# Kernel optimization log

Measured on AMD Instinct MI355X. Metric: run time of the kernel, lower is better.

## Reference

```python
import jax, jax.numpy as jnp
import numpy as np

DIM = 128
NUM_HEADS = 16
DPH = DIM // NUM_HEADS
N_ATOMS = 50000
N_EDGES = 400000
LN_EPS = 1e-5


def setup_inputs() -> dict:
    key = jax.random.key(0)
    ks = jax.random.split(key, 12)
    inp = {
        "node_feat": jax.random.normal(ks[0], (N_ATOMS, DIM), jnp.float32),
        "edge_feat": jax.random.normal(ks[1], (N_EDGES, NUM_HEADS, DPH), jnp.float32),
        "edge_vec": jax.random.normal(ks[2], (N_EDGES, 3, 1, 1), jnp.float32),
        "radial": jax.random.uniform(ks[3], (N_EDGES,), jnp.float32),
        "qkv_w": jax.random.normal(ks[4], (DIM, 3 * DIM), jnp.float32) / np.sqrt(DIM),
        "qkv_b": jnp.zeros((3 * DIM,), jnp.float32),
        "out_w": jax.random.normal(ks[5], (DIM, DIM), jnp.float32) / np.sqrt(DIM),
        "out_b": jnp.zeros((DIM,), jnp.float32),
        "ln_g": jnp.ones((DIM,), jnp.float32),
        "ln_b": jnp.zeros((DIM,), jnp.float32),
        "row": jax.random.randint(ks[6], (N_EDGES,), 0, N_ATOMS, jnp.int32),
        "col": jax.random.randint(ks[7], (N_EDGES,), 0, N_ATOMS, jnp.int32),
        "natoms": N_ATOMS,
    }
    return inp


def _layer_norm(x, g, b):
    mu = jnp.mean(x, axis=-1, keepdims=True)
    var = jnp.mean(jnp.square(x - mu), axis=-1, keepdims=True)
    return (x - mu) * jax.lax.rsqrt(var + LN_EPS) * g + b


def reference(node_feat, edge_feat, edge_vec, radial, qkv_w, qkv_b, out_w, out_b,
              ln_g, ln_b, row, col, natoms):
    # LayerNorm + QKV projection (dense)
    h = _layer_norm(node_feat, ln_g, ln_b)                     # [N, D]
    qkv = h @ qkv_w + qkv_b                                    # [N, 3D]
    qkv = qkv.reshape(-1, NUM_HEADS, 3 * DPH)                  # [N, H, 3*Dh]
    q, k, v = qkv[..., :DPH], qkv[..., DPH:2 * DPH], qkv[..., 2 * DPH:]
    # Gather by edge indices
    q_row, k_col, v_col = q[row], k[col], v[col]               # [E, H, Dh]
    # Per-edge attention (exact erf GELU, matching torch nn.GELU default)
    attn = jax.nn.gelu(jnp.sum(q_row * k_col, axis=-1), approximate=False)
    attn = attn * radial[:, None]                              # [E, H]
    # Scalar message + scatter-add
    m_feat = v_col * edge_feat * attn[..., None]               # [E, H, Dh]
    m_feat = jax.ops.segment_sum(m_feat, row, num_segments=natoms)
    m_feat = m_feat.reshape(natoms, DIM)                       # [N, D]
    # Vector message + scatter-add
    m_vec = v_col[:, None, :, :] * edge_vec                    # [E, 3, H, Dh]
    m_vec = jax.ops.segment_sum(m_vec, row, num_segments=natoms)
    delta_node_vec = m_vec.reshape(natoms, 3, DIM)             # [N, 3, D]
    delta_node_feat = m_feat @ out_w + out_b                   # [N, D]
    return delta_node_feat, delta_node_vec
```

## Files before the change

### kernel.cpp

```cpp
#include <hip/hip_runtime.h>
#include <math.h>

#define DIM 128
#define NHEADS 16
#define DPH 8
#define NATOMS 50000
#define NEDGES 400000
#define LN_EPS 1e-5f

typedef float f32x4 __attribute__((ext_vector_type(4)));
typedef short s16x8 __attribute__((ext_vector_type(8)));

static __device__ __forceinline__ unsigned short f2bf(float f) {
  unsigned u = __builtin_bit_cast(unsigned, f);
  unsigned r = (u + 0x7FFFu + ((u >> 16) & 1u)) >> 16;
  return (unsigned short)r;
}
static __device__ __forceinline__ unsigned packbf(float lo, float hi) {
  return (unsigned)f2bf(lo) | ((unsigned)f2bf(hi) << 16);
}
static __device__ __forceinline__ float bflo(unsigned u) {
  return __builtin_bit_cast(float, u << 16);
}
static __device__ __forceinline__ float bfhi(unsigned u) {
  return __builtin_bit_cast(float, u & 0xffff0000u);
}

static __device__ __forceinline__ float gelu_fast(float x) {
  const float c0 = 0.7978845608028654f;
  const float c1 = 0.044715f;
  float u = c0 * (x + c1 * x * x * x);
  return __fdividef(x, 1.0f + __expf(-2.0f * u));
}

#define HIST_NB ((NEDGES + 255) / 256)
#define SCAN_NB 196
#define LN_NB (NATOMS / 16)

__global__ __launch_bounds__(256) void k_convert(
    const float* __restrict__ qkv_w, const float* __restrict__ out_w,
    unsigned short* __restrict__ wTq, unsigned short* __restrict__ wTo,
    int* __restrict__ cnt)
{
  const int idx = blockIdx.x * 256 + threadIdx.x;
  if (idx < NATOMS) cnt[idx] = 0;
  if (idx < 384 * 128) {
    const int c = idx >> 7, k = idx & 127;
    wTq[idx] = f2bf(qkv_w[k * 384 + c]);
  } else {
    const int i2 = idx - 384 * 128;
    const int c = i2 >> 7, k = i2 & 127;
    wTo[i2] = f2bf(out_w[k * 128 + c]);
  }
}

__global__ __launch_bounds__(256) void k_ln_qkv_hist(
    const float* __restrict__ node, const unsigned short* __restrict__ wTq,
    const float* __restrict__ bias, const float* __restrict__ g,
    const float* __restrict__ beta, unsigned* __restrict__ qb,
    unsigned* __restrict__ kvb, const int* __restrict__ row,
    int* __restrict__ cnt)
{
  if (blockIdx.x >= LN_NB) {
    const int e = (blockIdx.x - LN_NB) * 256 + threadIdx.x;
    if (e < NEDGES) atomicAdd(&cnt[row[e]], 1);
    return;
  }

  __shared__ float hpad[16][132];
  __shared__ float so[16][388];
  const int a0 = blockIdx.x * 16;
  const int tid = threadIdx.x;
  const int wid = tid >> 6;
  const int lane = tid & 63;

  for (int j = 0; j < 4; ++j) {
    const int a = wid * 4 + j;
    const float x0 = node[(size_t)(a0 + a) * DIM + lane];
    const float x1 = node[(size_t)(a0 + a) * DIM + 64 + lane];
    float s = x0 + x1;
    #pragma unroll
    for (int m = 1; m < 64; m <<= 1) s += __shfl_xor(s, m);
    const float mu = s * (1.0f / 128.0f);
    const float d0 = x0 - mu, d1 = x1 - mu;
    float v = d0 * d0 + d1 * d1;
    #pragma unroll
    for (int m = 1; m < 64; m <<= 1) v += __shfl_xor(v, m);
    const float rs = rsqrtf(v * (1.0f / 128.0f) + LN_EPS);
    hpad[a][lane]      = d0 * rs * g[lane]      + beta[lane];
    hpad[a][64 + lane] = d1 * rs * g[64 + lane] + beta[64 + lane];
  }
  __syncthreads();

  const int lrow = lane & 15;
  const int lquad = lane >> 4;
  const int colbase = wid * 96;

  s16x8 afrag[4];
  #pragma unroll
  for (int ks = 0; ks < 4; ++ks) {
    const int koff = ks * 32 + lquad * 8;
    const float4 p0 = *reinterpret_cast<const float4*>(&hpad[lrow][koff]);
    const float4 p1 = *reinterpret_cast<const float4*>(&hpad[lrow][koff + 4]);
    s16x8 af;
    af[0] = (short)f2bf(p0.x); af[1] = (short)f2bf(p0.y);
    af[2] = (short)f2bf(p0.z); af[3] = (short)f2bf(p0.w);
    af[4] = (short)f2bf(p1.x); af[5] = (short)f2bf(p1.y);
    af[6] = (short)f2bf(p1.z); af[7] = (short)f2bf(p1.w);
    afrag[ks] = af;
  }

  f32x4 acc[6];
  #pragma unroll
  for (int tt = 0; tt < 6; ++tt) acc[tt] = (f32x4){0.f, 0.f, 0.f, 0.f};

  #pragma unroll
  for (int tt = 0; tt < 6; ++tt) {
    const int cg = colbase + tt * 16 + lrow;
    #pragma unroll
    for (int ks = 0; ks < 4; ++ks) {
      const s16x8 bf = *reinterpret_cast<const s16x8*>(
          &wTq[(size_t)cg * 128 + ks * 32 + lquad * 8]);
      acc[tt] = __builtin_amdgcn_mfma_f32_16x16x32_bf16(afrag[ks], bf, acc[tt], 0, 0, 0);
    }
  }

  #pragma unroll
  for (int tt = 0; tt < 6; ++tt) {
    const int cg = colbase + tt * 16 + lrow;
    const float bz = bias[cg];
    const int hj = cg / 24;
    const int off = cg - hj * 24;
    int moff;
    if (off < 8)       moff = hj * 8 + off;
    else if (off < 16) moff = 128 + (hj * 8 + off - 8) * 2;
    else               moff = 128 + (hj * 8 + off - 16) * 2 + 1;
    #pragma unroll
    for (int r = 0; r < 4; ++r)
      so[lquad * 4 + r][moff] = acc[tt][r] + bz;
  }
  __syncthreads();

  #pragma unroll
  for (int kk = 0; kk < 4; ++kk) {
    const int i = tid + kk * 256;
    const int rowi = i >> 6;
    const int c2 = i & 63;
    qb[(size_t)(a0 + rowi) * 64 + c2] =
        packbf(so[rowi][2 * c2], so[rowi][2 * c2 + 1]);
  }
  #pragma unroll
  for (int kk = 0; kk < 8; ++kk) {
    const int i = tid + kk * 256;
    const int rowi = i >> 7;
    const int c = i & 127;
    kvb[(size_t)(a0 + rowi) * 128 + c] =
        packbf(so[rowi][128 + 2 * c], so[rowi][128 + 2 * c + 1]);
  }
}

__global__ __launch_bounds__(256) void k_scan1(const int* __restrict__ cnt,
                                               int* __restrict__ locx,
                                               int* __restrict__ psum) {
  __shared__ int sh[256];
  const int tid = threadIdx.x;
  const int i = blockIdx.x * 256 + tid;
  const int v = (i < NATOMS) ? cnt[i] : 0;
  sh[tid] = v;
  __syncthreads();
  #pragma unroll
  for (int off = 1; off < 256; off <<= 1) {
    const int cur = sh[tid];
    const int add = (tid >= off) ? sh[tid - off] : 0;
    __syncthreads();
    sh[tid] = cur + add;
    __syncthreads();
  }
  if (i < NATOMS) locx[i] = sh[tid] - v;
  if (tid == 255) psum[blockIdx.x] = sh[255];
}

__global__ __launch_bounds__(256) void k_scan23(const int* __restrict__ psum,
                                                const int* __restrict__ locx,
                                                int* __restrict__ base,
                                                int* __restrict__ cursor) {
  __shared__ int ws[4];
  const int bid = blockIdx.x;
  const int tid = threadIdx.x;
  const int lane = tid & 63;
  const int wid = tid >> 6;

  int s = (tid < bid) ? psum[tid] : 0;
  #pragma unroll
  for (int m = 1; m < 64; m <<= 1) s += __shfl_xor(s, m);
  if (lane == 0) ws[wid] = s;
  __syncthreads();
  const int off = ws[0] + ws[1] + ws[2] + ws[3];

  const int i = bid * 256 + tid;
  if (i < NATOMS) {
    const int b = locx[i] + off;
    base[i] = b;
    cursor[i] = b;
  }
  if (bid == 0 && tid == 0) base[NATOMS] = NEDGES;
}

__global__ __launch_bounds__(256) void k_scatter(
    const int* __restrict__ row, const int* __restrict__ col,
    const float* __restrict__ radial, const float* __restrict__ evec,
    int* __restrict__ cursor, int4* __restrict__ descA,
    float2* __restrict__ descB)
{
  const int e = blockIdx.x * 256 + threadIdx.x;
  if (e < NEDGES) {
    const int p = atomicAdd(&cursor[row[e]], 1);
    descA[p] = make_int4(e, col[e], __float_as_int(radial[e]),
                         __float_as_int(evec[(size_t)e * 3]));
    descB[p] = make_float2(evec[(size_t)e * 3 + 1], evec[(size_t)e * 3 + 2]);
  }
}

__global__ __launch_bounds__(256) void k_edge_csr(
    const unsigned* __restrict__ qb, const uint2* __restrict__ kvb,
    const float2* __restrict__ ef2, const int4* __restrict__ descA,
    const float2* __restrict__ descB, const int* __restrict__ base,
    unsigned* __restrict__ mfeatw, float* __restrict__ outvec)
{
  const int tid = threadIdx.x;
  const int a = blockIdx.x * 4 + (tid >> 6);
  const int t = tid & 63;

  const int pBeg = __builtin_amdgcn_readfirstlane(base[a]);
  const int pEnd = __builtin_amdgcn_readfirstlane(base[a + 1]);
  const int deg = pEnd - pBeg;

  float f0 = 0.f, f1 = 0.f;
  float va0 = 0.f, va1 = 0.f, vb0 = 0.f, vb1 = 0.f, vc0 = 0.f, vc1 = 0.f;

  if (deg > 0) {
    const unsigned qp = qb[(size_t)a * 64 + t];
    const float q0 = bflo(qp), q1 = bfhi(qp);
    const int pLast = pEnd - 1;

    int4 u0, u1, u2, u3;
    float2 w0, w1, w2, w3;
    uint2 kvA0, kvA1, kvA2, kvA3, kvB0, kvB1, kvB2, kvB3,
          kvC0, kvC1, kvC2, kvC3;
    float2 efA0, efA1, efA2, efA3, efB0, efB1, efB2, efB3,
           efC0, efC1, efC2, efC3;
    float rA0, rA1, rA2, rA3, xA0, xA1, xA2, xA3,
          yA0, yA1, yA2, yA3, zA0, zA1, zA2, zA3;
    float rB0, rB1, rB2, rB3, xB0, xB1, xB2, xB3,
          yB0, yB1, yB2, yB3, zB0, zB1, zB2, zB3;
    float rC0, rC1, rC2, rC3, xC0, xC1, xC2, xC3,
          yC0, yC1, yC2, yC3, zC0, zC1, zC2, zC3;

#define LDESC(P) do {                                                       \
    const int j0_ = ((P)     <= pLast) ? (P)     : pLast;                   \
    const int j1_ = ((P) + 1 <= pLast) ? (P) + 1 : pLast;                   \
    const int j2_ = ((P) + 2 <= pLast) ? (P) + 2 : pLast;                   \
    const int j3_ = ((P) + 3 <= pLast) ? (P) + 3 : pLast;                   \
    u0 = descA[j0_]; w0 = descB[j0_];                                       \
    u1 = descA[j1_]; w1 = descB[j1_];                                       \
    u2 = descA[j2_]; w2 = descB[j2_];                                       \
    u3 = descA[j3_]; w3 = descB[j3_];                                       \
  } while (0)

#define STAGE(S, IT) do {                                                   \
    const bool g0_ = (IT)     < deg, g1_ = (IT) + 1 < deg;                  \
    const bool g2_ = (IT) + 2 < deg, g3_ = (IT) + 3 < deg;                  \
    r##S##0 = g0_ ? __int_as_float(u0.z) : 0.f;                             \
    x##S##0 = g0_ ? __int_as_float(u0.w) : 0.f;                             \
    y##S##0 = g0_ ? w0.x : 0.f;  z##S##0 = g0_ ? w0.y : 0.f;                \
    r##S##1 = g1_ ? __int_as_float(u1.z) : 0.f;                             \
    x##S##1 = g1_ ? __int_as_float(u1.w) : 0.f;                             \
    y##S##1 = g1_ ? w1.x : 0.f;  z##S##1 = g1_ ? w1.y : 0.f;                \
    r##S##2 = g2_ ? __int_as_float(u2.z) : 0.f;                             \
    x##S##2 = g2_ ? __int_as_float(u2.w) : 0.f;                             \
    y##S##2 = g2_ ? w2.x : 0.f;  z##S##2 = g2_ ? w2.y : 0.f;                \
    r##S##3 = g3_ ? __int_as_float(u3.z) : 0.f;                             \
    x##S##3 = g3_ ? __int_as_float(u3.w) : 0.f;                             \
    y##S##3 = g3_ ? w3.x : 0.f;  z##S##3 = g3_ ? w3.y : 0.f;                \
    kv##S##0 = kvb[(size_t)(unsigned)u0.y * 64 + t];                        \
    ef##S##0 = ef2[(size_t)(unsigned)u0.x * 64 + t];                        \
    kv##S##1 = kvb[(size_t)(unsigned)u1.y * 64 + t];                        \
    ef##S##1 = ef2[(size_t)(unsigned)u1.x * 64 + t];                        \
    kv##S##2 = kvb[(size_t)(unsigned)u2.y * 64 + t];                        \
    ef##S##2 = ef2[(size_t)(unsigned)u2.x * 64 + t];                        \
    kv##S##3 = kvb[(size_t)(unsigned)u3.y * 64 + t];                        \
    ef##S##3 = ef2[(size_t)(unsigned)u3.x * 64 + t];                        \
  } while (0)

#define EDGE1(KV, EF, RR, XX, YY, ZZ) do {                                  \
    const float kx0_ = bflo(KV.x), kx1_ = bflo(KV.y);                       \
    const float vx0_ = bfhi(KV.x), vx1_ = bfhi(KV.y);                       \
    float pd_ = q0 * kx0_; pd_ = fmaf(q1, kx1_, pd_);                       \
    pd_ += __shfl_xor(pd_, 1); pd_ += __shfl_xor(pd_, 2);                   \
    const float at_ = gelu_fast(pd_) * (RR);                                \
    f0 = fmaf(vx0_ * EF.x, at_, f0);                                        \
    f1 = fmaf(vx1_ * EF.y, at_, f1);                                        \
    va0 = fmaf(vx0_, (XX), va0); va1 = fmaf(vx1_, (XX), va1);               \
    vb0 = fmaf(vx0_, (YY), vb0); vb1 = fmaf(vx1_, (YY), vb1);               \
    vc0 = fmaf(vx0_, (ZZ), vc0); vc1 = fmaf(vx1_, (ZZ), vc1);               \
  } while (0)

#define COMPUTE(S) do {                                                     \
    EDGE1(kv##S##0, ef##S##0, r##S##0, x##S##0, y##S##0, z##S##0);          \
    EDGE1(kv##S##1, ef##S##1, r##S##1, x##S##1, y##S##1, z##S##1);          \
    EDGE1(kv##S##2, ef##S##2, r##S##2, x##S##2, y##S##2, z##S##2);          \
    EDGE1(kv##S##3, ef##S##3, r##S##3, x##S##3, y##S##3, z##S##3);          \
  } while (0)

    LDESC(pBeg);      STAGE(A, 0);
    LDESC(pBeg + 4);  STAGE(B, 4);
    LDESC(pBeg + 8);  STAGE(C, 8);
    LDESC(pBeg + 12);

    int it = 0;
    while (true) {
      COMPUTE(A);
      if (it + 4 >= deg) break;
      STAGE(A, it + 12); LDESC(pBeg + it + 16);
      COMPUTE(B);
      if (it + 8 >= deg) break;
      STAGE(B, it + 16); LDESC(pBeg + it + 20);
      COMPUTE(C);
      if (it + 12 >= deg) break;
      STAGE(C, it + 20); LDESC(pBeg + it + 24);
      it += 12;
    }

#undef LDESC
#undef STAGE
#undef EDGE1
#undef COMPUTE
  }

  mfeatw[(size_t)a * 64 + t] = packbf(f0, f1);
  float* ov = outvec + (size_t)a * 384 + 2 * t;
  *reinterpret_cast<float2*>(ov)       = make_float2(va0, va1);
  *reinterpret_cast<float2*>(ov + 128) = make_float2(vb0, vb1);
  *reinterpret_cast<float2*>(ov + 256) = make_float2(vc0, vc1);
}

__global__ __launch_bounds__(256) void k_out(
    const unsigned short* __restrict__ mfeatb,
    const unsigned short* __restrict__ wTo,
    const float* __restrict__ bias, float* __restrict__ out)
{
  __shared__ float so[16][132];
  const int a0 = blockIdx.x * 16;
  const int tid = threadIdx.x;
  const int wid = tid >> 6;
  const int lane = tid & 63;
  const int lrow = lane & 15;
  const int lquad = lane >> 4;

  s16x8 afrag[4];
  #pragma unroll
  for (int ks = 0; ks < 4; ++ks)
    afrag[ks] = *reinterpret_cast<const s16x8*>(
        &mfeatb[(size_t)(a0 + lrow) * 128 + ks * 32 + lquad * 8]);

  f32x4 acc[2];
  acc[0] = (f32x4){0.f, 0.f, 0.f, 0.f};
  acc[1] = (f32x4){0.f, 0.f, 0.f, 0.f};

  #pragma unroll
  for (int tt = 0; tt < 2; ++tt) {
    const int cg = wid * 32 + tt * 16 + lrow;
    #pragma unroll
    for (int ks = 0; ks < 4; ++ks) {
      const s16x8 bf = *reinterpret_cast<const s16x8*>(
          &wTo[(size_t)cg * 128 + ks * 32 + lquad * 8]);
      acc[tt] = __builtin_amdgcn_mfma_f32_16x16x32_bf16(afrag[ks], bf, acc[tt], 0, 0, 0);
    }
  }

  #pragma unroll
  for (int tt = 0; tt < 2; ++tt) {
    const int cg = wid * 32 + tt * 16 + lrow;
    const float bz = bias[cg];
    #pragma unroll
    for (int r = 0; r < 4; ++r)
      so[lquad * 4 + r][cg] = acc[tt][r] + bz;
  }
  __syncthreads();

  f32x4* out4 = (f32x4*)out;
  #pragma unroll
  for (int kk = 0; kk < 2; ++kk) {
    const int idx4 = tid + kk * 256;
    const int rowi = idx4 >> 5;
    const int c4 = idx4 & 31;
    out4[(size_t)(a0 + rowi) * 32 + c4] =
        *reinterpret_cast<const f32x4*>(&so[rowi][c4 * 4]);
  }
}

extern "C" void kernel_launch(void* const* d_in, const int* in_sizes, int n_in,
                              void* d_out, int out_size, void* d_ws, size_t ws_size,
                              hipStream_t stream) {
  const float* node_feat = (const float*)d_in[0];
  const float* edge_feat = (const float*)d_in[1];
  const float* edge_vec  = (const float*)d_in[2];
  const float* radial    = (const float*)d_in[3];
  const float* qkv_w     = (const float*)d_in[4];
  const float* qkv_b     = (const float*)d_in[5];
  const float* out_w     = (const float*)d_in[6];
  const float* out_b     = (const float*)d_in[7];
  const float* ln_g      = (const float*)d_in[8];
  const float* ln_b      = (const float*)d_in[9];
  const int*   row       = (const int*)d_in[10];
  const int*   col       = (const int*)d_in[11];

  float* out      = (float*)d_out;
  float* out_feat = out;
  float* out_vec  = out + (size_t)NATOMS * DIM;

  unsigned* qb  = (unsigned*)d_ws;
  unsigned* kvb = qb + (size_t)NATOMS * 64;
  unsigned short* mfeatb = (unsigned short*)(kvb + (size_t)NATOMS * 128);
  unsigned short* wTq = mfeatb + (size_t)NATOMS * 128;
  unsigned short* wTo = wTq + 384 * 128;
  int4* descA  = (int4*)(wTo + 128 * 128);
  float2* descB = (float2*)(descA + NEDGES);
  int* cnt    = (int*)(descB + NEDGES);
  int* base   = cnt + NATOMS;
  int* cursor = base + NATOMS + 1;
  int* locx   = cursor + NATOMS;
  int* psum   = locx + NATOMS;

  k_convert<<<256, 256, 0, stream>>>(qkv_w, out_w, wTq, wTo, cnt);

  k_ln_qkv_hist<<<LN_NB + HIST_NB, 256, 0, stream>>>(
      node_feat, wTq, qkv_b, ln_g, ln_b, qb, kvb, row, cnt);

  k_scan1<<<SCAN_NB, 256, 0, stream>>>(cnt, locx, psum);
  k_scan23<<<SCAN_NB, 256, 0, stream>>>(psum, locx, base, cursor);
  k_scatter<<<HIST_NB, 256, 0, stream>>>(row, col, radial, edge_vec, cursor,
                                         descA, descB);

  k_edge_csr<<<NATOMS / 4, 256, 0, stream>>>(
      qb, (const uint2*)kvb, (const float2*)edge_feat, descA, descB, base,
      (unsigned*)mfeatb, out_vec);

  k_out<<<NATOMS / 16, 256, 0, stream>>>(mfeatb, wTo, out_b, out_feat);
}
```

Measured before the change: 217.9 us.

## Fuse output projection into edge CSR kernel epilogue with FP32 FMA

Removes the separate k_out MFMA kernel and the bf16 mfeat workspace. Each edge-kernel block now stages its four atoms' aggregated features in shared memory, synchronises, and computes the 128x128 output projection with scalar FP32 FMAs, reading out_w directly from global memory. This saves a kernel launch, the mfeat write and re-read, and the out_w transpose and convert. In exchange every block re-reads the full weight matrix through the cache, and the block-wide barrier makes waves with short edge lists wait for the slowest one.

```diff
diff --git a/kernel.cpp b/kernel.cpp
--- a/kernel.cpp
+++ b/kernel.cpp
@@ -38,8 +38,7 @@
 #define LN_NB (NATOMS / 16)
 
 __global__ __launch_bounds__(256) void k_convert(
-    const float* __restrict__ qkv_w, const float* __restrict__ out_w,
-    unsigned short* __restrict__ wTq, unsigned short* __restrict__ wTo,
+    const float* __restrict__ qkv_w, unsigned short* __restrict__ wTq,
     int* __restrict__ cnt)
 {
   const int idx = blockIdx.x * 256 + threadIdx.x;
@@ -47,10 +46,6 @@
   if (idx < 384 * 128) {
     const int c = idx >> 7, k = idx & 127;
     wTq[idx] = f2bf(qkv_w[k * 384 + c]);
-  } else {
-    const int i2 = idx - 384 * 128;
-    const int c = i2 >> 7, k = i2 & 127;
-    wTo[i2] = f2bf(out_w[k * 128 + c]);
   }
 }
 
@@ -225,10 +220,13 @@
     const unsigned* __restrict__ qb, const uint2* __restrict__ kvb,
     const float2* __restrict__ ef2, const int4* __restrict__ descA,
     const float2* __restrict__ descB, const int* __restrict__ base,
-    unsigned* __restrict__ mfeatw, float* __restrict__ outvec)
+    const float* __restrict__ outw, const float* __restrict__ outb,
+    float* __restrict__ outfeat, float* __restrict__ outvec)
 {
+  __shared__ float sm[4][128];
   const int tid = threadIdx.x;
-  const int a = blockIdx.x * 4 + (tid >> 6);
+  const int wv = tid >> 6;
+  const int a = blockIdx.x * 4 + wv;
   const int t = tid & 63;
 
   const int pBeg = __builtin_amdgcn_readfirstlane(base[a]);
@@ -337,66 +335,27 @@
 #undef COMPUTE
   }
 
-  mfeatw[(size_t)a * 64 + t] = packbf(f0, f1);
   float* ov = outvec + (size_t)a * 384 + 2 * t;
   *reinterpret_cast<float2*>(ov)       = make_float2(va0, va1);
   *reinterpret_cast<float2*>(ov + 128) = make_float2(vb0, vb1);
   *reinterpret_cast<float2*>(ov + 256) = make_float2(vc0, vc1);
-}
-
-__global__ __launch_bounds__(256) void k_out(
-    const unsigned short* __restrict__ mfeatb,
-    const unsigned short* __restrict__ wTo,
-    const float* __restrict__ bias, float* __restrict__ out)
-{
-  __shared__ float so[16][132];
-  const int a0 = blockIdx.x * 16;
-  const int tid = threadIdx.x;
-  const int wid = tid >> 6;
-  const int lane = tid & 63;
-  const int lrow = lane & 15;
-  const int lquad = lane >> 4;
-
-  s16x8 afrag[4];
-  #pragma unroll
-  for (int ks = 0; ks < 4; ++ks)
-    afrag[ks] = *reinterpret_cast<const s16x8*>(
-        &mfeatb[(size_t)(a0 + lrow) * 128 + ks * 32 + lquad * 8]);
-
-  f32x4 acc[2];
-  acc[0] = (f32x4){0.f, 0.f, 0.f, 0.f};
-  acc[1] = (f32x4){0.f, 0.f, 0.f, 0.f};
-
-  #pragma unroll
-  for (int tt = 0; tt < 2; ++tt) {
-    const int cg = wid * 32 + tt * 16 + lrow;
-    #pragma unroll
-    for (int ks = 0; ks < 4; ++ks) {
-      const s16x8 bf = *reinterpret_cast<const s16x8*>(
-          &wTo[(size_t)cg * 128 + ks * 32 + lquad * 8]);
-      acc[tt] = __builtin_amdgcn_mfma_f32_16x16x32_bf16(afrag[ks], bf, acc[tt], 0, 0, 0);
-    }
-  }
-
-  #pragma unroll
-  for (int tt = 0; tt < 2; ++tt) {
-    const int cg = wid * 32 + tt * 16 + lrow;
-    const float bz = bias[cg];
-    #pragma unroll
-    for (int r = 0; r < 4; ++r)
-      so[lquad * 4 + r][cg] = acc[tt][r] + bz;
-  }
+  sm[wv][2 * t]     = f0;
+  sm[wv][2 * t + 1] = f1;
   __syncthreads();
 
-  f32x4* out4 = (f32x4*)out;
-  #pragma unroll
-  for (int kk = 0; kk < 2; ++kk) {
-    const int idx4 = tid + kk * 256;
-    const int rowi = idx4 >> 5;
-    const int c4 = idx4 & 31;
-    out4[(size_t)(a0 + rowi) * 32 + c4] =
-        *reinterpret_cast<const f32x4*>(&so[rowi][c4 * 4]);
-  }
+  const int c = tid & 127;
+  const int ap = tid >> 7;
+  const float bz = outb[c];
+  float acc0 = bz, acc1 = bz;
+  #pragma unroll 8
+  for (int k = 0; k < 128; ++k) {
+    const float wk = outw[k * 128 + c];
+    acc0 = fmaf(sm[2 * ap][k], wk, acc0);
+    acc1 = fmaf(sm[2 * ap + 1][k], wk, acc1);
+  }
+  const size_t aa = (size_t)(blockIdx.x * 4 + 2 * ap) * 128 + c;
+  outfeat[aa] = acc0;
+  outfeat[aa + 128] = acc1;
 }
 
 extern "C" void kernel_launch(void* const* d_in, const int* in_sizes, int n_in,
@@ -421,10 +380,8 @@
 
   unsigned* qb  = (unsigned*)d_ws;
   unsigned* kvb = qb + (size_t)NATOMS * 64;
-  unsigned short* mfeatb = (unsigned short*)(kvb + (size_t)NATOMS * 128);
-  unsigned short* wTq = mfeatb + (size_t)NATOMS * 128;
-  unsigned short* wTo = wTq + 384 * 128;
-  int4* descA  = (int4*)(wTo + 128 * 128);
+  unsigned short* wTq = (unsigned short*)(kvb + (size_t)NATOMS * 128);
+  int4* descA  = (int4*)(wTq + 384 * 128);
   float2* descB = (float2*)(descA + NEDGES);
   int* cnt    = (int*)(descB + NEDGES);
   int* base   = cnt + NATOMS;
@@ -432,7 +389,7 @@
   int* locx   = cursor + NATOMS;
   int* psum   = locx + NATOMS;
 
-  k_convert<<<256, 256, 0, stream>>>(qkv_w, out_w, wTq, wTo, cnt);
+  k_convert<<<SCAN_NB, 256, 0, stream>>>(qkv_w, wTq, cnt);
 
   k_ln_qkv_hist<<<LN_NB + HIST_NB, 256, 0, stream>>>(
       node_feat, wTq, qkv_b, ln_g, ln_b, qb, kvb, row, cnt);
@@ -444,7 +401,5 @@
 
   k_edge_csr<<<NATOMS / 4, 256, 0, stream>>>(
       qb, (const uint2*)kvb, (const float2*)edge_feat, descA, descB, base,
-      (unsigned*)mfeatb, out_vec);
-
-  k_out<<<NATOMS / 16, 256, 0, stream>>>(mfeatb, wTo, out_b, out_feat);
-}
+      out_w, out_b, out_feat, out_vec);
+}
```

New measurement: 275.8 us. +26.6%, slower.
